# Kernel tuning notes

Hardware: AMD Instinct MI355X
Metric: run time of the kernel (lower is better)

## Reference

```python
import jax, jax.numpy as jnp
import numpy as np

ALPHA = 0.2  # tf.nn.leaky_relu default alpha
B, LATENT, T, N = 8, 256, 128, 768
F, L, E = 4, 3, 12288


def _causal_conv1d(x, w, b):
    # x: [B,T,Cin], w: [K,Cin,Cout] -> causal pad left by K-1
    k = w.shape[0]
    y = jax.lax.conv_general_dilated(x, w, (1,), ((k - 1, 0),),
                                     dimension_numbers=('NWC', 'WIO', 'NWC'))
    return y + b


def _same_conv1d(x, w, b):
    y = jax.lax.conv_general_dilated(x, w, (1,), 'SAME',
                                     dimension_numbers=('NWC', 'WIO', 'NWC'))
    return y + b


def _same_conv2d(x, w, b):
    y = jax.lax.conv_general_dilated(x, w, (1, 1), 'SAME',
                                     dimension_numbers=('NHWC', 'HWIO', 'NHWC'))
    return y + b


def _gat(nodes, row, col, qw, qb, kw, kb, vw, vb):
    # tf_geometric-style single-head GAT; row/col already contain self-loops.
    M = nodes.shape[0]
    Q = jax.nn.leaky_relu(nodes @ qw + qb, ALPHA)
    K = jax.nn.leaky_relu(nodes @ kw + kb, ALPHA)
    V = nodes @ vw
    scale = jnp.sqrt(jnp.asarray(Q.shape[-1], nodes.dtype))
    score = jnp.sum(Q[row] * K[col], axis=-1) / scale  # [E']
    smax = jax.ops.segment_max(score, row, num_segments=M)
    ex = jnp.exp(score - smax[row])
    den = jax.ops.segment_sum(ex, row, num_segments=M)
    att = ex / den[row]
    out = jax.ops.segment_sum(V[col] * att[:, None], row, num_segments=M)
    return out + vb


def _gw_layer(y, row, col, wa, ba, wb, bb, qw, qb, kw, kb, vw, vb, rw, rb):
    b_, t_, n_, f_ = y.shape
    x = jnp.moveaxis(y, -1, 0)  # [F,B,T,N]

    def branch(xf, wa_, ba_, wb_, bb_, qw_, qb_, kw_, kb_, vw_, vb_):
        a = jax.nn.sigmoid(_causal_conv1d(xf, wa_, ba_))
        g = a * jnp.tanh(_causal_conv1d(xf, wb_, bb_))   # gated TCN [B,T,N]
        nodes = g.transpose(0, 2, 1).reshape(b_ * n_, t_)  # node id = b*N + n
        h = _gat(nodes, row, col, qw_, qb_, kw_, kb_, vw_, vb_)
        return h.reshape(b_, n_, t_).transpose(0, 2, 1)  # [B,T,N]

    outs = jax.vmap(branch)(x, wa, ba, wb, bb, qw, qb, kw, kb, vw, vb)
    outs = jnp.moveaxis(outs, 0, -1)                      # [B,T,N,F]
    res = jnp.einsum('btnf,fg->btng', y, rw) + rb         # 1x1 res conv
    return outs + res


def _decoder(x, edges, shunt_dense_w, shunt_dense_b, shunt_c1_w, shunt_c1_b,
             shunt_c2_w, shunt_c2_b, tcn_a_w, tcn_a_b, tcn_b_w, tcn_b_b,
             gat_q_w, gat_q_b, gat_k_w, gat_k_b, gat_v_w, gat_v_b,
             res_w, res_b, skip_w, skip_b, out1_w, out1_b, out2_w, out2_b):
    # ConvShunt: [B,latent] -> [B,T] -> [B,T,N] -> [B,T,N,F]
    y = x @ shunt_dense_w + shunt_dense_b
    y = _same_conv1d(y[..., None], shunt_c1_w, shunt_c1_b)
    y = _same_conv2d(y[..., None], shunt_c2_w, shunt_c2_b)
    M = B * N
    self_idx = jnp.arange(M, dtype=edges.dtype)
    row = jnp.concatenate([edges[0], self_idx])
    col = jnp.concatenate([edges[1], self_idx])
    skips = []
    for i in range(L):
        y = _gw_layer(y, row, col, tcn_a_w[i], tcn_a_b[i], tcn_b_w[i], tcn_b_b[i],
                      gat_q_w[i], gat_q_b[i], gat_k_w[i], gat_k_b[i],
                      gat_v_w[i], gat_v_b[i], res_w[i], res_b[i])
        skips.append(jax.nn.leaky_relu(
            jnp.einsum('btnf,f->btn', y, skip_w[i]) + skip_b[i], ALPHA))
    s = jnp.stack(skips, axis=-1)                         # [B,T,N,L]
    g = jax.nn.leaky_relu(_same_conv2d(s, out1_w, out1_b), ALPHA)
    return _same_conv2d(g, out2_w, out2_b)                # [B,T,N,1]


def setup_inputs() -> dict:
    ks = iter(jax.random.split(jax.random.key(0), 32))

    def w(shape, fan_in):
        return jax.random.normal(next(ks), shape, jnp.float32) / np.sqrt(fan_in).astype(np.float32)

    return {
        'x': jax.random.normal(next(ks), (B, LATENT), jnp.float32),
        'edges': jax.random.randint(next(ks), (2, E), 0, N, jnp.int32),
        'shunt_dense_w': w((LATENT, T), LATENT),
        'shunt_dense_b': jnp.zeros((T,), jnp.float32),
        'shunt_c1_w': w((3, 1, N), 3),
        'shunt_c1_b': jnp.zeros((N,), jnp.float32),
        'shunt_c2_w': w((3, 3, 1, F), 9),
        'shunt_c2_b': jnp.zeros((F,), jnp.float32),
        'tcn_a_w': w((L, F, 5, N, N), 5 * N),
        'tcn_a_b': jnp.zeros((L, F, N), jnp.float32),
        'tcn_b_w': w((L, F, 5, N, N), 5 * N),
        'tcn_b_b': jnp.zeros((L, F, N), jnp.float32),
        'gat_q_w': w((L, F, T, T), T),
        'gat_q_b': jnp.zeros((L, F, T), jnp.float32),
        'gat_k_w': w((L, F, T, T), T),
        'gat_k_b': jnp.zeros((L, F, T), jnp.float32),
        'gat_v_w': w((L, F, T, T), T),
        'gat_v_b': jnp.zeros((L, F, T), jnp.float32),
        'res_w': w((L, F, F), F),
        'res_b': jnp.zeros((L, F), jnp.float32),
        'skip_w': w((L, F), F),
        'skip_b': jnp.zeros((L,), jnp.float32),
        'out1_w': w((3, 3, L, 1), 9 * L),
        'out1_b': jnp.zeros((1,), jnp.float32),
        'out2_w': w((1, 1, 1, 1), 1),
        'out2_b': jnp.zeros((1,), jnp.float32),
    }


def reference(x, edges, shunt_dense_w, shunt_dense_b, shunt_c1_w, shunt_c1_b,
              shunt_c2_w, shunt_c2_b, tcn_a_w, tcn_a_b, tcn_b_w, tcn_b_b,
              gat_q_w, gat_q_b, gat_k_w, gat_k_b, gat_v_w, gat_v_b,
              res_w, res_b, skip_w, skip_b, out1_w, out1_b, out2_w, out2_b):
    return _decoder(x, edges, shunt_dense_w, shunt_dense_b, shunt_c1_w, shunt_c1_b,
                    shunt_c2_w, shunt_c2_b, tcn_a_w, tcn_a_b, tcn_b_w, tcn_b_b,
                    gat_q_w, gat_q_b, gat_k_w, gat_k_b, gat_v_w, gat_v_b,
                    res_w, res_b, skip_w, skip_b, out1_w, out1_b, out2_w, out2_b)
```

## Files before the change

kernel.cpp:

```cpp
#include <hip/hip_runtime.h>
#include <math.h>

#define ALPHA_ 0.2f
#define AS1 __attribute__((address_space(1)))
#define AS3 __attribute__((address_space(3)))

constexpr int B_ = 8, LATENT_ = 256, T_ = 128, N_ = 768, F_ = 4, L_ = 3, E_ = 12288;
constexpr int M_ = B_ * N_;
constexpr int MT_ = B_ * T_;
constexpr int EP_ = E_ + M_;
constexpr int BTN_ = B_ * T_ * N_;
constexpr size_t SZ_ = (size_t)BTN_ * F_;
constexpr int KTCN_ = 5 * N_;
constexpr int KS4_ = KTCN_ / 4;
constexpr int TP_ = T_ + 4;

typedef __bf16 bf16x8 __attribute__((ext_vector_type(8)));
typedef float f32x4 __attribute__((ext_vector_type(4)));

__device__ __forceinline__ float lrelu(float x) { return x > 0.0f ? x : ALPHA_ * x; }
__device__ __forceinline__ unsigned short f2bf(float x) {
    union { __bf16 h; unsigned short u; } c; c.h = (__bf16)x; return c.u;
}
__device__ __forceinline__ float bf2f(unsigned short u) {
    return __uint_as_float(((unsigned)u) << 16);
}

__global__ void k_dense(const float* __restrict__ x, const float* __restrict__ w,
                        const float* __restrict__ b, float* __restrict__ y0) {
    int i = blockIdx.x * blockDim.x + threadIdx.x;
    if (i >= B_ * T_) return;
    int bb = i / T_, t = i % T_;
    float acc = b[t];
    for (int l = 0; l < LATENT_; ++l) acc += x[bb * LATENT_ + l] * w[l * T_ + t];
    y0[i] = acc;
}

__global__ void k_conv1(const float* __restrict__ y0, const float* __restrict__ w,
                        const float* __restrict__ b, float* __restrict__ y1) {
    int i = blockIdx.x * blockDim.x + threadIdx.x;
    if (i >= BTN_) return;
    int n = i % N_, t = (i / N_) % T_, bb = i / (N_ * T_);
    float acc = b[n];
    #pragma unroll
    for (int k = 0; k < 3; ++k) {
        int tt = t - 1 + k;
        if (tt >= 0 && tt < T_) acc += y0[bb * T_ + tt] * w[k * N_ + n];
    }
    y1[i] = acc;
}

__global__ void k_conv2w(const float* __restrict__ y1, const float* __restrict__ w,
                         const float* __restrict__ b, float* __restrict__ y,
                         unsigned short* __restrict__ xTpad) {
    int i = blockIdx.x * blockDim.x + threadIdx.x;
    if (i >= BTN_) return;
    int n = i % N_, t = (i / N_) % T_, bb = i / (N_ * T_);
    float acc[F_];
    #pragma unroll
    for (int f = 0; f < F_; ++f) acc[f] = b[f];
    #pragma unroll
    for (int dt = 0; dt < 3; ++dt) {
        int tt = t - 1 + dt;
        if (tt < 0 || tt >= T_) continue;
        #pragma unroll
        for (int dn = 0; dn < 3; ++dn) {
            int nn = n - 1 + dn;
            if (nn < 0 || nn >= N_) continue;
            float v = y1[(bb * T_ + tt) * N_ + nn];
            #pragma unroll
            for (int f = 0; f < F_; ++f) acc[f] += v * w[(dt * 3 + dn) * F_ + f];
        }
    }
    #pragma unroll
    for (int f = 0; f < F_; ++f) {
        y[(size_t)i * F_ + f] = acc[f];
        xTpad[((size_t)(f * B_ + bb) * TP_ + 4 + t) * N_ + n] = f2bf(acc[f]);
    }
}

__global__ __launch_bounds__(256) void k_convT2(const float* __restrict__ aw,
        const float* __restrict__ bw, unsigned short* __restrict__ wat3,
        unsigned short* __restrict__ wbt3) {
    __shared__ float tl[64 * 65];
    const int z = blockIdx.z;
    const int f = z & 3, wsel = (z >> 2) & 1, layer = z >> 3;
    const size_t toff = ((size_t)layer * F_ + f) * (size_t)KTCN_ * N_;
    const float* in = (wsel ? bw : aw) + toff;
    unsigned short* outT = (wsel ? wbt3 : wat3) + toff;
    const int n0 = blockIdx.x * 64, k0 = blockIdx.y * 64;
    const int tid = threadIdx.x;
    const int lr = tid >> 4;
    const int lc4 = (tid & 15) * 4;
    #pragma unroll
    for (int r = 0; r < 4; ++r) {
        const int k = lr + r * 16;
        const float4 v = *(const float4*)(in + (size_t)(k0 + k) * N_ + n0 + lc4);
        tl[k * 65 + lc4 + 0] = v.x;
        tl[k * 65 + lc4 + 1] = v.y;
        tl[k * 65 + lc4 + 2] = v.z;
        tl[k * 65 + lc4 + 3] = v.w;
    }
    __syncthreads();
    const int sr = tid >> 3;
    const int sc8 = (tid & 7) * 8;
    #pragma unroll
    for (int r = 0; r < 2; ++r) {
        const int n = sr + r * 32;
        unsigned short pk[8];
        #pragma unroll
        for (int i = 0; i < 8; ++i) pk[i] = f2bf(tl[(sc8 + i) * 65 + n]);
        *(uint4*)(outT + (size_t)(n0 + n) * KTCN_ + k0 + sc8) = *(uint4*)pk;
    }
}

__global__ __launch_bounds__(256) void k_convTproj(const float* __restrict__ qw,
        const float* __restrict__ kw, const float* __restrict__ vw,
        unsigned short* __restrict__ pwt3) {
    __shared__ float tl[32][33];
    const int z = blockIdx.z;
    const int f = z & 3;
    const int sel = (z >> 2) % 3;
    const int layer = z / 12;
    const float* in = (sel == 0 ? qw : (sel == 1 ? kw : vw))
                      + ((size_t)layer * F_ + f) * T_ * T_;
    unsigned short* outT = pwt3 + (((size_t)layer * 3 + sel) * F_ + f) * T_ * T_;
    const int x0 = blockIdx.x * 32;
    const int y0 = blockIdx.y * 32;
    const int tx = threadIdx.x & 31, ty = threadIdx.x >> 5;
    #pragma unroll
    for (int r = 0; r < 4; ++r)
        tl[ty + r * 8][tx] = in[(size_t)(y0 + ty + r * 8) * T_ + x0 + tx];
    __syncthreads();
    #pragma unroll
    for (int r = 0; r < 4; ++r)
        outT[(size_t)(x0 + ty + r * 8) * T_ + y0 + tx] = f2bf(tl[tx][ty + r * 8]);
}

__global__ __launch_bounds__(256) void k_tcn_mfma(
        const unsigned short* __restrict__ xTpad,
        const unsigned short* __restrict__ wat, const unsigned short* __restrict__ wbt,
        const float* __restrict__ ba, const float* __restrict__ bbias,
        unsigned short* __restrict__ pa, unsigned short* __restrict__ pb) {
    __shared__ unsigned short As[128 * 32];
    __shared__ unsigned short Bs[128 * 32];
    const int bid = blockIdx.x;
    const int bt = bid / 192;
    const int c = bid - bt * 192;
    const int xb = c % 6;
    const int zz = c / 6;
    const int f = zz & 3;
    const int wsel = (zz >> 2) & 1;
    const int s = zz >> 3;
    const int n0 = xb * 128;
    const unsigned short* xf = xTpad + (size_t)(f * B_ + bt) * TP_ * N_;
    const unsigned short* wf = (wsel ? wbt : wat) + (size_t)f * N_ * KTCN_ + (size_t)n0 * KTCN_;
    const float* bias = (wsel ? bbias : ba) + f * N_;
    unsigned short* out = (wsel ? pb : pa) + (size_t)s * SZ_;
    const int tid = threadIdx.x;
    const int lane = tid & 63;
    const int w = tid >> 6;
    const int wm = (w >> 1) * 64, wn = (w & 1) * 64;
    const int r16 = lane & 15, kb = lane >> 4;
    const int srow = lane >> 2;
    const int scol = (((lane & 3) ^ ((lane >> 3) & 3)) * 8);
    const int kx = (kb ^ ((r16 >> 1) & 3)) * 8;
    f32x4 acc[4][4] = {};
    const int k_lo = s * KS4_, k_hi = k_lo + KS4_;
    for (int kk0 = k_lo; kk0 < k_hi; kk0 += 32) {
        const int ks = kk0 / N_;
        const int nin0 = kk0 - ks * N_;
        #pragma unroll
        for (int h = 0; h < 2; ++h) {
            const int seg = w + 4 * h;
            const int row = seg * 16 + srow;
            const unsigned short* gA = xf + (size_t)(row + ks) * N_ + nin0 + scol;
            const unsigned short* gB = wf + (size_t)row * KTCN_ + kk0 + scol;
            __builtin_amdgcn_global_load_lds((const AS1 unsigned int*)(const void*)gA,
                    (AS3 unsigned int*)(void*)(As + seg * 512), 16, 0, 0);
            __builtin_amdgcn_global_load_lds((const AS1 unsigned int*)(const void*)gB,
                    (AS3 unsigned int*)(void*)(Bs + seg * 512), 16, 0, 0);
        }
        __syncthreads();
        bf16x8 av[4], bv[4];
        #pragma unroll
        for (int i = 0; i < 4; ++i) av[i] = *(const bf16x8*)(As + (wm + i * 16 + r16) * 32 + kx);
        #pragma unroll
        for (int j = 0; j < 4; ++j) bv[j] = *(const bf16x8*)(Bs + (wn + j * 16 + r16) * 32 + kx);
        #pragma unroll
        for (int i = 0; i < 4; ++i)
            #pragma unroll
            for (int j = 0; j < 4; ++j)
                acc[i][j] = __builtin_amdgcn_mfma_f32_16x16x32_bf16(av[i], bv[j], acc[i][j], 0, 0, 0);
        __syncthreads();
    }
    unsigned short* of = out + (size_t)(f * B_ + bt) * T_ * N_;
    #pragma unroll
    for (int i = 0; i < 4; ++i) {
        #pragma unroll
        for (int j = 0; j < 4; ++j) {
            const int n = n0 + wn + j * 16 + r16;
            const float bv2 = (s == 0) ? bias[n] : 0.0f;
            #pragma unroll
            for (int r = 0; r < 4; ++r) {
                const int m = wm + i * 16 + kb * 4 + r;
                of[(size_t)m * N_ + n] = f2bf(acc[i][j][r] + bv2);
            }
        }
    }
}

__global__ __launch_bounds__(256) void k_gate_nodes(const unsigned short* __restrict__ pa,
        const unsigned short* __restrict__ pb, unsigned short* __restrict__ nodes) {
    __shared__ float tl[32][33];
    const int bz = blockIdx.z;
    const int t0 = blockIdx.x * 32, n0 = blockIdx.y * 32;
    const int tx = threadIdx.x & 31, ty = threadIdx.x >> 5;
    const size_t base = (size_t)bz * T_ * N_;
    #pragma unroll
    for (int r = 0; r < 4; ++r) {
        const size_t idx = base + (size_t)(t0 + ty + r * 8) * N_ + n0 + tx;
        float av = 0.0f, bvv = 0.0f;
        #pragma unroll
        for (int s = 0; s < 4; ++s) {
            av += bf2f(pa[(size_t)s * SZ_ + idx]);
            bvv += bf2f(pb[(size_t)s * SZ_ + idx]);
        }
        tl[ty + r * 8][tx] = (1.0f / (1.0f + __expf(-av))) * tanhf(bvv);
    }
    __syncthreads();
    #pragma unroll
    for (int r = 0; r < 4; ++r)
        nodes[base + (size_t)(n0 + ty + r * 8) * T_ + t0 + tx] = f2bf(tl[tx][ty + r * 8]);
}

__global__ __launch_bounds__(256) void k_proj_mfma(
        const unsigned short* __restrict__ nodes, const unsigned short* __restrict__ pwt,
        const float* __restrict__ qb, const float* __restrict__ kbias,
        unsigned short* __restrict__ Q, unsigned short* __restrict__ K,
        unsigned short* __restrict__ V) {
    __shared__ unsigned short As[128 * 32];
    __shared__ unsigned short Bs[128 * 32];
    const int zz = blockIdx.z;
    const int f = zz & 3;
    const int sel = zz >> 2;
    const int m0 = blockIdx.y * 128;
    const unsigned short* af = nodes + (size_t)f * M_ * T_;
    const unsigned short* wfp = pwt + (size_t)sel * F_ * T_ * T_ + (size_t)f * T_ * T_;
    const float* bias = (sel == 0) ? qb : (sel == 1 ? kbias : nullptr);
    unsigned short* out = (sel == 0) ? Q : (sel == 1 ? K : V);
    const int tid = threadIdx.x;
    const int lane = tid & 63;
    const int w = tid >> 6;
    const int wm = (w >> 1) * 64, wn = (w & 1) * 64;
    const int r16 = lane & 15, kb = lane >> 4;
    const int srow = lane >> 2;
    const int scol = (((lane & 3) ^ ((lane >> 3) & 3)) * 8);
    const int kx = (kb ^ ((r16 >> 1) & 3)) * 8;
    f32x4 acc[4][4] = {};
    for (int kk0 = 0; kk0 < T_; kk0 += 32) {
        #pragma unroll
        for (int h = 0; h < 2; ++h) {
            const int seg = w + 4 * h;
            const int row = seg * 16 + srow;
            const unsigned short* gA = af + (size_t)(m0 + row) * T_ + kk0 + scol;
            const unsigned short* gB = wfp + (size_t)row * T_ + kk0 + scol;
            __builtin_amdgcn_global_load_lds((const AS1 unsigned int*)(const void*)gA,
                    (AS3 unsigned int*)(void*)(As + seg * 512), 16, 0, 0);
            __builtin_amdgcn_global_load_lds((const AS1 unsigned int*)(const void*)gB,
                    (AS3 unsigned int*)(void*)(Bs + seg * 512), 16, 0, 0);
        }
        __syncthreads();
        bf16x8 av[4], bv[4];
        #pragma unroll
        for (int i = 0; i < 4; ++i) av[i] = *(const bf16x8*)(As + (wm + i * 16 + r16) * 32 + kx);
        #pragma unroll
        for (int j = 0; j < 4; ++j) bv[j] = *(const bf16x8*)(Bs + (wn + j * 16 + r16) * 32 + kx);
        #pragma unroll
        for (int i = 0; i < 4; ++i)
            #pragma unroll
            for (int j = 0; j < 4; ++j)
                acc[i][j] = __builtin_amdgcn_mfma_f32_16x16x32_bf16(av[i], bv[j], acc[i][j], 0, 0, 0);
        __syncthreads();
    }
    const int do_l = (sel < 2);
    unsigned short* of = out + (size_t)f * M_ * T_;
    #pragma unroll
    for (int i = 0; i < 4; ++i) {
        #pragma unroll
        for (int j = 0; j < 4; ++j) {
            const int n = wn + j * 16 + r16;
            #pragma unroll
            for (int r = 0; r < 4; ++r) {
                const int m = m0 + wm + i * 16 + kb * 4 + r;
                float v = acc[i][j][r];
                if (bias) v += bias[f * T_ + n];
                if (do_l) v = lrelu(v);
                of[(size_t)m * T_ + n] = f2bf(v);
            }
        }
    }
}

__device__ __forceinline__ int edge_row(const int* e, int i) { return i < E_ ? e[i] : i - E_; }
__device__ __forceinline__ int edge_col(const int* e, int i) { return i < E_ ? e[E_ + i] : i - E_; }

__global__ void k_hist(const int* __restrict__ edges, int* __restrict__ deg) {
    int i = blockIdx.x * blockDim.x + threadIdx.x;
    if (i >= EP_) return;
    atomicAdd(&deg[edge_row(edges, i)], 1);
}

__global__ __launch_bounds__(256) void k_scan(const int* __restrict__ deg,
        int* __restrict__ rowptr, int* __restrict__ cursor) {
    __shared__ int part[256];
    const int tid = threadIdx.x;
    constexpr int PER = M_ / 256;
    int loc[PER];
    int s = 0;
    #pragma unroll
    for (int j = 0; j < PER; ++j) { loc[j] = s; s += deg[tid * PER + j]; }
    part[tid] = s;
    __syncthreads();
    if (tid == 0) {
        int run = 0;
        for (int i2 = 0; i2 < 256; ++i2) { int v = part[i2]; part[i2] = run; run += v; }
        rowptr[M_] = run;
    }
    __syncthreads();
    const int off = part[tid];
    #pragma unroll
    for (int j = 0; j < PER; ++j) {
        rowptr[tid * PER + j] = off + loc[j];
        cursor[tid * PER + j] = off + loc[j];
    }
}

__global__ void k_scatter(const int* __restrict__ edges, int* __restrict__ cursor,
                          int* __restrict__ csr_col) {
    int i = blockIdx.x * blockDim.x + threadIdx.x;
    if (i >= EP_) return;
    int r = edge_row(edges, i), c = edge_col(edges, i);
    int pos = atomicAdd(&cursor[r], 1);
    csr_col[pos] = c;
}

__global__ __launch_bounds__(256) void k_gat(const unsigned short* __restrict__ Q,
        const unsigned short* __restrict__ Kb, const unsigned short* __restrict__ V,
        const int* __restrict__ rowptr, const int* __restrict__ csr_col,
        unsigned short* __restrict__ H) {
    constexpr int CAP = 128;
    __shared__ float sc[4][CAP];
    const int w = threadIdx.x >> 6, lane = threadIdx.x & 63;
    const int wv = blockIdx.x * 4 + w;
    const int f = wv / M_, r = wv - f * M_;
    const int p0 = rowptr[r], p1 = rowptr[r + 1];
    const unsigned short* Qr = Q + ((size_t)f * M_ + r) * T_;
    const float q0 = bf2f(Qr[lane]), q1 = bf2f(Qr[lane + 64]);
    float mx = -3.4e38f;
    for (int j = p0; j < p1; ++j) {
        const unsigned short* Kc = Kb + ((size_t)f * M_ + csr_col[j]) * T_;
        float s = q0 * bf2f(Kc[lane]) + q1 * bf2f(Kc[lane + 64]);
        #pragma unroll
        for (int mk = 32; mk >= 1; mk >>= 1) s += __shfl_xor(s, mk);
        s *= 0.0883883476483184f;
        if (lane == 0 && j - p0 < CAP) sc[w][j - p0] = s;
        mx = fmaxf(mx, s);
    }
    float den = 0.0f;
    for (int j = p0; j < p1; ++j) {
        float s;
        if (j - p0 < CAP) s = sc[w][j - p0];
        else {
            const unsigned short* Kc = Kb + ((size_t)f * M_ + csr_col[j]) * T_;
            s = q0 * bf2f(Kc[lane]) + q1 * bf2f(Kc[lane + 64]);
            #pragma unroll
            for (int mk = 32; mk >= 1; mk >>= 1) s += __shfl_xor(s, mk);
            s *= 0.0883883476483184f;
        }
        den += __expf(s - mx);
    }
    const float rden = 1.0f / den;
    float a0 = 0.0f, a1 = 0.0f;
    for (int j = p0; j < p1; ++j) {
        const int c = csr_col[j];
        float s;
        if (j - p0 < CAP) s = sc[w][j - p0];
        else {
            const unsigned short* Kc = Kb + ((size_t)f * M_ + c) * T_;
            s = q0 * bf2f(Kc[lane]) + q1 * bf2f(Kc[lane + 64]);
            #pragma unroll
            for (int mk = 32; mk >= 1; mk >>= 1) s += __shfl_xor(s, mk);
            s *= 0.0883883476483184f;
        }
        const float att = __expf(s - mx) * rden;
        const unsigned short* Vc = V + ((size_t)f * M_ + c) * T_;
        a0 += att * bf2f(Vc[lane]);
        a1 += att * bf2f(Vc[lane + 64]);
    }
    unsigned short* Hr = H + ((size_t)f * M_ + r) * T_;
    Hr[lane] = f2bf(a0);
    Hr[lane + 64] = f2bf(a1);
}

__global__ __launch_bounds__(256) void k_combine_t(const float* __restrict__ y,
        const unsigned short* __restrict__ H, const float* __restrict__ vb,
        const float* __restrict__ rw, const float* __restrict__ rb,
        const float* __restrict__ skw, const float* __restrict__ skb, int layer,
        float* __restrict__ ynext, unsigned short* __restrict__ xTpad,
        float* __restrict__ sbufp) {
    __shared__ float hl[F_][32][33];
    const int b = blockIdx.z;
    const int t0 = blockIdx.x * 32, n0 = blockIdx.y * 32;
    const int tx = threadIdx.x & 31, ty = threadIdx.x >> 5;
    #pragma unroll
    for (int g = 0; g < F_; ++g)
        #pragma unroll
        for (int r = 0; r < 4; ++r) {
            const int nn = ty + r * 8;
            hl[g][nn][tx] = bf2f(H[((size_t)g * M_ + b * N_ + n0 + nn) * T_ + t0 + tx]);
        }
    __syncthreads();
    #pragma unroll
    for (int r = 0; r < 4; ++r) {
        const int tt = ty + r * 8;
        const int t = t0 + tt;
        const size_t i = ((size_t)b * T_ + t) * N_ + n0 + tx;
        const float4 y4 = *(const float4*)(y + i * 4);
        float o[F_];
        #pragma unroll
        for (int g = 0; g < F_; ++g) {
            float acc = hl[g][tx][tt] + vb[g * T_ + t] + rb[g];
            acc += y4.x * rw[0 * F_ + g] + y4.y * rw[1 * F_ + g]
                 + y4.z * rw[2 * F_ + g] + y4.w * rw[3 * F_ + g];
            o[g] = acc;
        }
        float4 o4 = {o[0], o[1], o[2], o[3]};
        *(float4*)(ynext + i * 4) = o4;
        #pragma unroll
        for (int g = 0; g < F_; ++g)
            xTpad[((size_t)(g * B_ + b) * TP_ + 4 + t) * N_ + n0 + tx] = f2bf(o[g]);
        float sk = skb[layer];
        #pragma unroll
        for (int g = 0; g < F_; ++g) sk += o[g] * skw[layer * F_ + g];
        sbufp[(size_t)layer * BTN_ + i] = lrelu(sk);
    }
}

__global__ void k_final(const float* __restrict__ sbufp, const float* __restrict__ o1w,
        const float* __restrict__ o1b, const float* __restrict__ o2w,
        const float* __restrict__ o2b, float* __restrict__ out) {
    int i = blockIdx.x * blockDim.x + threadIdx.x;
    if (i >= BTN_) return;
    int n = i % N_, t = (i / N_) % T_, bb = i / (N_ * T_);
    float acc = o1b[0];
    #pragma unroll
    for (int dt = 0; dt < 3; ++dt) {
        int tt = t - 1 + dt;
        if (tt < 0 || tt >= T_) continue;
        #pragma unroll
        for (int dn = 0; dn < 3; ++dn) {
            int nn = n - 1 + dn;
            if (nn < 0 || nn >= N_) continue;
            const size_t base = (size_t)(bb * T_ + tt) * N_ + nn;
            #pragma unroll
            for (int l = 0; l < L_; ++l)
                acc += sbufp[(size_t)l * BTN_ + base] * o1w[(dt * 3 + dn) * L_ + l];
        }
    }
    float g = lrelu(acc);
    out[i] = g * o2w[0] + o2b[0];
}

extern "C" void kernel_launch(void* const* d_in, const int* in_sizes, int n_in,
                              void* d_out, int out_size, void* d_ws, size_t ws_size,
                              hipStream_t stream) {
    const float* x       = (const float*)d_in[0];
    const int*   edges   = (const int*)d_in[1];
    const float* sd_w    = (const float*)d_in[2];
    const float* sd_b    = (const float*)d_in[3];
    const float* c1w     = (const float*)d_in[4];
    const float* c1b     = (const float*)d_in[5];
    const float* c2w     = (const float*)d_in[6];
    const float* c2b     = (const float*)d_in[7];
    const float* tcn_a_w = (const float*)d_in[8];
    const float* tcn_a_b = (const float*)d_in[9];
    const float* tcn_b_w = (const float*)d_in[10];
    const float* tcn_b_b = (const float*)d_in[11];
    const float* gat_q_w = (const float*)d_in[12];
    const float* gat_q_b = (const float*)d_in[13];
    const float* gat_k_w = (const float*)d_in[14];
    const float* gat_k_b = (const float*)d_in[15];
    const float* gat_v_w = (const float*)d_in[16];
    const float* gat_v_b = (const float*)d_in[17];
    const float* res_w   = (const float*)d_in[18];
    const float* res_b   = (const float*)d_in[19];
    const float* skip_w  = (const float*)d_in[20];
    const float* skip_b  = (const float*)d_in[21];
    const float* out1_w  = (const float*)d_in[22];
    const float* out1_b  = (const float*)d_in[23];
    const float* out2_w  = (const float*)d_in[24];
    const float* out2_b  = (const float*)d_in[25];
    float* out = (float*)d_out;

    float* ws = (float*)d_ws;
    size_t off = 0;
    auto alloc = [&](size_t nf) { float* p = ws + off; off += nf; return p; };
    float* ybuf  = alloc(SZ_);
    float* y2buf = alloc(SZ_);
    float* sbufp = alloc((size_t)BTN_ * L_);
    float* y0    = alloc(MT_);
    float* y1    = alloc(BTN_);
    unsigned short* xTpad  = (unsigned short*)alloc((size_t)F_ * B_ * TP_ * N_ / 2 + 16);
    unsigned short* nodesb = (unsigned short*)alloc(SZ_ / 2);
    unsigned short* qb16   = (unsigned short*)alloc(SZ_ / 2);
    unsigned short* kb16   = (unsigned short*)alloc(SZ_ / 2);
    unsigned short* vb16   = (unsigned short*)alloc(SZ_ / 2);
    unsigned short* Hb     = (unsigned short*)alloc(SZ_ / 2);
    unsigned short* pa     = (unsigned short*)alloc(SZ_ * 2);
    unsigned short* pb     = (unsigned short*)alloc(SZ_ * 2);
    unsigned short* wat3 = (unsigned short*)alloc((size_t)L_ * F_ * KTCN_ * N_ / 2);
    unsigned short* wbt3 = (unsigned short*)alloc((size_t)L_ * F_ * KTCN_ * N_ / 2);
    unsigned short* pwt3 = (unsigned short*)alloc((size_t)L_ * 3 * F_ * T_ * T_ / 2);
    int* rowptr  = (int*)alloc(M_ + 1);
    int* cursor  = (int*)alloc(M_);
    int* deg     = (int*)alloc(M_);
    int* csr_col = (int*)alloc(EP_);
    (void)ws_size; (void)in_sizes; (void)n_in; (void)out_size;

    hipMemsetAsync(xTpad, 0, (size_t)F_ * B_ * TP_ * N_ * 2, stream);
    hipMemsetAsync(deg, 0, M_ * 4, stream);
    k_hist<<<(EP_ + 255) / 256, 256, 0, stream>>>(edges, deg);
    k_scan<<<1, 256, 0, stream>>>(deg, rowptr, cursor);
    k_scatter<<<(EP_ + 255) / 256, 256, 0, stream>>>(edges, cursor, csr_col);

    dim3 gw2(N_ / 64, KTCN_ / 64, 8 * L_);
    k_convT2<<<gw2, 256, 0, stream>>>(tcn_a_w, tcn_b_w, wat3, wbt3);
    dim3 gpw(T_ / 32, T_ / 32, 12 * L_);
    k_convTproj<<<gpw, 256, 0, stream>>>(gat_q_w, gat_k_w, gat_v_w, pwt3);

    k_dense<<<(B_ * T_ + 255) / 256, 256, 0, stream>>>(x, sd_w, sd_b, y0);
    k_conv1<<<(BTN_ + 255) / 256, 256, 0, stream>>>(y0, c1w, c1b, y1);
    k_conv2w<<<(BTN_ + 255) / 256, 256, 0, stream>>>(y1, c2w, c2b, ybuf, xTpad);

    float* cur = ybuf;
    float* nxt = y2buf;
    for (int layer = 0; layer < L_; ++layer) {
        const float* ba = tcn_a_b + (size_t)layer * F_ * N_;
        const float* bb = tcn_b_b + (size_t)layer * F_ * N_;
        const float* qb = gat_q_b + (size_t)layer * F_ * T_;
        const float* kbias = gat_k_b + (size_t)layer * F_ * T_;
        const float* vb = gat_v_b + (size_t)layer * F_ * T_;
        const float* rw = res_w + (size_t)layer * F_ * F_;
        const float* rb = res_b + (size_t)layer * F_;
        const unsigned short* wat = wat3 + (size_t)layer * F_ * KTCN_ * N_;
        const unsigned short* wbt = wbt3 + (size_t)layer * F_ * KTCN_ * N_;
        const unsigned short* pwt = pwt3 + (size_t)layer * 3 * F_ * T_ * T_;

        k_tcn_mfma<<<1536, 256, 0, stream>>>(xTpad, wat, wbt, ba, bb, pa, pb);
        dim3 gg(T_ / 32, N_ / 32, F_ * B_);
        k_gate_nodes<<<gg, 256, 0, stream>>>(pa, pb, nodesb);
        dim3 gp(1, M_ / 128, 12);
        k_proj_mfma<<<gp, 256, 0, stream>>>(nodesb, pwt, qb, kbias, qb16, kb16, vb16);
        k_gat<<<(F_ * M_) / 4, 256, 0, stream>>>(qb16, kb16, vb16, rowptr, csr_col, Hb);
        dim3 gc(T_ / 32, N_ / 32, B_);
        k_combine_t<<<gc, 256, 0, stream>>>(cur, Hb, vb, rw, rb, skip_w, skip_b,
                layer, nxt, xTpad, sbufp);
        float* tmp = cur; cur = nxt; nxt = tmp;
    }
    k_final<<<(BTN_ + 255) / 256, 256, 0, stream>>>(sbufp, out1_w, out1_b, out2_w, out2_b, out);
}
```

Measured before the change: 610.6 us.

## Halve TCN split-K factor and retile weight transpose with bf16 swizzled LDS

The TCN MFMA GEMM now splits K into 2 chunks instead of 4. That halves the grid to 768 blocks, halves the bf16 partial-sum buffers, and cuts the gate kernel's partial reads from 8 to 4 per element. The weight transpose kernel now converts to bf16 before storing to LDS, tiles 256 K rows per block with an XOR swizzle, and writes 16-byte vectors per row. The trade-off is fewer, longer TCN blocks and so less parallelism across the GPU, in exchange for less partial-sum traffic.

```diff
diff --git a/kernel.cpp b/kernel.cpp
--- a/kernel.cpp
+++ b/kernel.cpp
@@ -12,7 +12,7 @@
 constexpr int BTN_ = B_ * T_ * N_;
 constexpr size_t SZ_ = (size_t)BTN_ * F_;
 constexpr int KTCN_ = 5 * N_;
-constexpr int KS4_ = KTCN_ / 4;
+constexpr int KSPLIT_ = KTCN_ / 2;
 constexpr int TP_ = T_ + 4;
 
 typedef __bf16 bf16x8 __attribute__((ext_vector_type(8)));
@@ -82,35 +82,37 @@
 __global__ __launch_bounds__(256) void k_convT2(const float* __restrict__ aw,
         const float* __restrict__ bw, unsigned short* __restrict__ wat3,
         unsigned short* __restrict__ wbt3) {
-    __shared__ float tl[64 * 65];
+    __shared__ unsigned short tl[64 * 256];
     const int z = blockIdx.z;
     const int f = z & 3, wsel = (z >> 2) & 1, layer = z >> 3;
     const size_t toff = ((size_t)layer * F_ + f) * (size_t)KTCN_ * N_;
     const float* in = (wsel ? bw : aw) + toff;
     unsigned short* outT = (wsel ? wbt3 : wat3) + toff;
-    const int n0 = blockIdx.x * 64, k0 = blockIdx.y * 64;
+    const int n0 = blockIdx.x * 64, k0 = blockIdx.y * 256;
     const int tid = threadIdx.x;
     const int lr = tid >> 4;
     const int lc4 = (tid & 15) * 4;
     #pragma unroll
-    for (int r = 0; r < 4; ++r) {
-        const int k = lr + r * 16;
+    for (int p = 0; p < 16; ++p) {
+        const int k = p * 16 + lr;
         const float4 v = *(const float4*)(in + (size_t)(k0 + k) * N_ + n0 + lc4);
-        tl[k * 65 + lc4 + 0] = v.x;
-        tl[k * 65 + lc4 + 1] = v.y;
-        tl[k * 65 + lc4 + 2] = v.z;
-        tl[k * 65 + lc4 + 3] = v.w;
+        const float vv[4] = {v.x, v.y, v.z, v.w};
+        #pragma unroll
+        for (int i = 0; i < 4; ++i) {
+            const int n = lc4 + i;
+            const int kk = k ^ (((n >> 2) & 7) << 3);
+            tl[n * 256 + kk] = f2bf(vv[i]);
+        }
     }
     __syncthreads();
-    const int sr = tid >> 3;
-    const int sc8 = (tid & 7) * 8;
-    #pragma unroll
-    for (int r = 0; r < 2; ++r) {
-        const int n = sr + r * 32;
-        unsigned short pk[8];
-        #pragma unroll
-        for (int i = 0; i < 8; ++i) pk[i] = f2bf(tl[(sc8 + i) * 65 + n]);
-        *(uint4*)(outT + (size_t)(n0 + n) * KTCN_ + k0 + sc8) = *(uint4*)pk;
+    const int rn = tid >> 5;
+    const int rc = tid & 31;
+    #pragma unroll
+    for (int q = 0; q < 8; ++q) {
+        const int n = q * 8 + rn;
+        const int kk = (rc * 8) ^ (((n >> 2) & 7) << 3);
+        const uint4 val = *(const uint4*)&tl[n * 256 + kk];
+        *(uint4*)(outT + (size_t)(n0 + n) * KTCN_ + k0 + rc * 8) = val;
     }
 }
 
@@ -145,8 +147,8 @@
     __shared__ unsigned short As[128 * 32];
     __shared__ unsigned short Bs[128 * 32];
     const int bid = blockIdx.x;
-    const int bt = bid / 192;
-    const int c = bid - bt * 192;
+    const int bt = bid / 96;
+    const int c = bid - bt * 96;
     const int xb = c % 6;
     const int zz = c / 6;
     const int f = zz & 3;
@@ -166,7 +168,7 @@
     const int scol = (((lane & 3) ^ ((lane >> 3) & 3)) * 8);
     const int kx = (kb ^ ((r16 >> 1) & 3)) * 8;
     f32x4 acc[4][4] = {};
-    const int k_lo = s * KS4_, k_hi = k_lo + KS4_;
+    const int k_lo = s * KSPLIT_, k_hi = k_lo + KSPLIT_;
     for (int kk0 = k_lo; kk0 < k_hi; kk0 += 32) {
         const int ks = kk0 / N_;
         const int nin0 = kk0 - ks * N_;
@@ -220,12 +222,8 @@
     #pragma unroll
     for (int r = 0; r < 4; ++r) {
         const size_t idx = base + (size_t)(t0 + ty + r * 8) * N_ + n0 + tx;
-        float av = 0.0f, bvv = 0.0f;
-        #pragma unroll
-        for (int s = 0; s < 4; ++s) {
-            av += bf2f(pa[(size_t)s * SZ_ + idx]);
-            bvv += bf2f(pb[(size_t)s * SZ_ + idx]);
-        }
+        const float av = bf2f(pa[idx]) + bf2f(pa[SZ_ + idx]);
+        const float bvv = bf2f(pb[idx]) + bf2f(pb[SZ_ + idx]);
         tl[ty + r * 8][tx] = (1.0f / (1.0f + __expf(-av))) * tanhf(bvv);
     }
     __syncthreads();
@@ -517,8 +515,8 @@
     unsigned short* kb16   = (unsigned short*)alloc(SZ_ / 2);
     unsigned short* vb16   = (unsigned short*)alloc(SZ_ / 2);
     unsigned short* Hb     = (unsigned short*)alloc(SZ_ / 2);
-    unsigned short* pa     = (unsigned short*)alloc(SZ_ * 2);
-    unsigned short* pb     = (unsigned short*)alloc(SZ_ * 2);
+    unsigned short* pa     = (unsigned short*)alloc(SZ_);
+    unsigned short* pb     = (unsigned short*)alloc(SZ_);
     unsigned short* wat3 = (unsigned short*)alloc((size_t)L_ * F_ * KTCN_ * N_ / 2);
     unsigned short* wbt3 = (unsigned short*)alloc((size_t)L_ * F_ * KTCN_ * N_ / 2);
     unsigned short* pwt3 = (unsigned short*)alloc((size_t)L_ * 3 * F_ * T_ * T_ / 2);
@@ -534,7 +532,7 @@
     k_scan<<<1, 256, 0, stream>>>(deg, rowptr, cursor);
     k_scatter<<<(EP_ + 255) / 256, 256, 0, stream>>>(edges, cursor, csr_col);
 
-    dim3 gw2(N_ / 64, KTCN_ / 64, 8 * L_);
+    dim3 gw2(N_ / 64, KTCN_ / 256, 8 * L_);
     k_convT2<<<gw2, 256, 0, stream>>>(tcn_a_w, tcn_b_w, wat3, wbt3);
     dim3 gpw(T_ / 32, T_ / 32, 12 * L_);
     k_convTproj<<<gpw, 256, 0, stream>>>(gat_q_w, gat_k_w, gat_v_w, pwt3);
@@ -557,7 +555,7 @@
         const unsigned short* wbt = wbt3 + (size_t)layer * F_ * KTCN_ * N_;
         const unsigned short* pwt = pwt3 + (size_t)layer * 3 * F_ * T_ * T_;
 
-        k_tcn_mfma<<<1536, 256, 0, stream>>>(xTpad, wat, wbt, ba, bb, pa, pb);
+        k_tcn_mfma<<<768, 256, 0, stream>>>(xTpad, wat, wbt, ba, bb, pa, pb);
         dim3 gg(T_ / 32, N_ / 32, F_ * B_);
         k_gate_nodes<<<gg, 256, 0, stream>>>(pa, pb, nodesb);
         dim3 gp(1, M_ / 128, 12);
```

Result: faster. 574.2 us (-6.0%).
